# Performance work log

Measured on AMD Instinct MI355X. Metric: run time of the kernel, lower is better.

Reference implementation:

```python
import jax, jax.numpy as jnp
import numpy as np

NUM_HEADS = 8
MODEL_DIM = 1024
SEQ_LEN = 2048


def setup_inputs() -> dict:
    key = jax.random.key(0)
    ks = jax.random.split(key, 9)
    H, D, L = NUM_HEADS, MODEL_DIM, SEQ_LEN
    s_in = 1.0 / np.sqrt(D)
    s_out = 1.0 / np.sqrt(H * D)
    return {
        "tokens": jax.random.normal(ks[0], (D, L), dtype=jnp.float32),
        "Wq": jax.random.uniform(ks[1], (H * D, D), jnp.float32, -s_in, s_in),
        "bq": jax.random.uniform(ks[2], (H * D,), jnp.float32, -s_in, s_in),
        "Wk": jax.random.uniform(ks[3], (H * D, D), jnp.float32, -s_in, s_in),
        "bk": jax.random.uniform(ks[4], (H * D,), jnp.float32, -s_in, s_in),
        "Wv": jax.random.uniform(ks[5], (H * D, D), jnp.float32, -s_in, s_in),
        "bv": jax.random.uniform(ks[6], (H * D,), jnp.float32, -s_in, s_in),
        "Wo": jax.random.uniform(ks[7], (D, H * D), jnp.float32, -s_out, s_out),
        "bo": jax.random.uniform(ks[8], (D,), jnp.float32, -s_out, s_out),
    }


def _split_heads(x, H, D, L):
    # Faithful to torch: raw .view of contiguous [H*D, L] into (L, H, D),
    # then permute(1, 2, 0) -> (H, D, L). This is a memory reinterpretation,
    # not a transpose, exactly as in the original module.
    return x.reshape(L, H, D).transpose(1, 2, 0)


def reference(tokens, Wq, bq, Wk, bk, Wv, bv, Wo, bo):
    D, L = tokens.shape
    H = Wq.shape[0] // D
    # 1x1 Conv1d == matmul over channel dim
    q = _split_heads(Wq @ tokens + bq[:, None], H, D, L)  # (H, D, L)
    k = _split_heads(Wk @ tokens + bk[:, None], H, D, L)  # (H, D, L)
    v = _split_heads(Wv @ tokens + bv[:, None], H, D, L)  # (H, D, L)
    scores = jnp.einsum("hdl,hdm->hlm", q, k) / np.sqrt(D)  # (H, L, L)
    # torch F.softmax without dim on a 3D tensor -> dim=0 (head axis)
    attn = jax.nn.softmax(scores, axis=0)
    ctx = jnp.einsum("hlm,hdm->hdl", attn, v)  # (H, D, L)
    out = Wo @ ctx.reshape(H * D, L) + bo[:, None]  # (D, L)
    return out
```

## Files before the change

### kernel.cpp

```cpp
#include <hip/hip_runtime.h>

#define SEQL 2048
#define DMODEL 1024
#define HDIM 8192

typedef unsigned short bf16_t;
typedef __attribute__((ext_vector_type(8))) short bf16x8;
typedef __attribute__((ext_vector_type(4))) float f32x4;

__device__ __forceinline__ bf16_t f2bf(float f) {
  unsigned u = __float_as_uint(f);
  u += 0x7fffu + ((u >> 16) & 1u);
  return (bf16_t)(u >> 16);
}
__device__ __forceinline__ float bf2f(bf16_t b) {
  return __uint_as_float(((unsigned)b) << 16);
}
__device__ __forceinline__ void st(bf16_t* p, float v) { *p = f2bf(v); }
__device__ __forceinline__ void st(float* p, float v) { *p = v; }

__global__ __launch_bounds__(256) void cvt_f32_bf16(const float* __restrict__ in,
                                                    bf16_t* __restrict__ out, int n) {
  int i = (blockIdx.x * 256 + threadIdx.x) * 4;
  if (i >= n) return;
  float4 f = *reinterpret_cast<const float4*>(in + i);
  ushort4 u;
  u.x = f2bf(f.x); u.y = f2bf(f.y); u.z = f2bf(f.z); u.w = f2bf(f.w);
  *reinterpret_cast<ushort4*>(out + i) = u;
}

__global__ __launch_bounds__(256) void transpose_cvt(const float* __restrict__ in,
                                                     bf16_t* __restrict__ out) {
  __shared__ float tile[32][33];
  int bx = blockIdx.x * 32;
  int by = blockIdx.y * 32;
  int tx = threadIdx.x, ty = threadIdx.y;
#pragma unroll
  for (int i = ty; i < 32; i += 8)
    tile[i][tx] = in[(size_t)(by + i) * SEQL + bx + tx];
  __syncthreads();
#pragma unroll
  for (int i = ty; i < 32; i += 8)
    out[(size_t)(bx + i) * DMODEL + by + tx] = f2bf(tile[tx][i]);
}

__global__ __launch_bounds__(256) void vsplit_k(const bf16_t* __restrict__ Vm,
                                                bf16_t* __restrict__ Vs) {
  __shared__ bf16_t tile[32][33];
  int h = blockIdx.z, h2 = h >> 1, r = h & 1;
  int m0 = blockIdx.x * 32, d0 = blockIdx.y * 32;
  int tx = threadIdx.x, ty = threadIdx.y;
#pragma unroll
  for (int i = ty; i < 32; i += 8)
    tile[i][tx] = Vm[(size_t)(4 * (m0 + i) + h2) * SEQL + r * DMODEL + d0 + tx];
  __syncthreads();
#pragma unroll
  for (int i = ty; i < 32; i += 8)
    Vs[((size_t)h * DMODEL + d0 + i) * SEQL + m0 + tx] = tile[tx][i];
}

__global__ __launch_bounds__(256) void softmax_heads(bf16_t* __restrict__ S) {
  const size_t HS = (size_t)SEQL * SEQL;
  size_t p = ((size_t)blockIdx.x * 256 + threadIdx.x) * 8;
  float v[8][8];
#pragma unroll
  for (int h = 0; h < 8; ++h) {
    bf16x8 x = *reinterpret_cast<const bf16x8*>(S + h * HS + p);
#pragma unroll
    for (int e = 0; e < 8; ++e) v[h][e] = bf2f((bf16_t)x[e]);
  }
#pragma unroll
  for (int e = 0; e < 8; ++e) {
    float mx = v[0][e];
#pragma unroll
    for (int h = 1; h < 8; ++h) mx = fmaxf(mx, v[h][e]);
    float s = 0.f;
#pragma unroll
    for (int h = 0; h < 8; ++h) { v[h][e] = __expf(v[h][e] - mx); s += v[h][e]; }
    float inv = 1.0f / s;
#pragma unroll
    for (int h = 0; h < 8; ++h) v[h][e] *= inv;
  }
#pragma unroll
  for (int h = 0; h < 8; ++h) {
    bf16x8 x;
#pragma unroll
    for (int e = 0; e < 8; ++e) x[e] = (short)f2bf(v[h][e]);
    *reinterpret_cast<bf16x8*>(S + h * HS + p) = x;
  }
}

__global__ __launch_bounds__(256) void reduce_out(const float* __restrict__ P,
                                                  const float* __restrict__ bo,
                                                  float* __restrict__ out) {
  const size_t NEL = (size_t)DMODEL * SEQL;
  size_t i = ((size_t)blockIdx.x * 256 + threadIdx.x) * 4;
  float4 a = *reinterpret_cast<const float4*>(P + i);
#pragma unroll
  for (int z = 1; z < 8; ++z) {
    float4 b = *reinterpret_cast<const float4*>(P + z * NEL + i);
    a.x += b.x; a.y += b.y; a.z += b.z; a.w += b.w;
  }
  float bias = bo[i / SEQL];
  a.x += bias; a.y += bias; a.z += bias; a.w += bias;
  *reinterpret_cast<float4*>(out + i) = a;
}

template <typename OutT, bool HAS_BIAS>
__global__ __launch_bounds__(512, 2) void gemm256(
    const bf16_t* __restrict__ A, const bf16_t* __restrict__ B,
    OutT* __restrict__ C, const float* __restrict__ bias,
    int M, int N, int K, int lda, int ldb, int ldc,
    long long sA, long long sB, long long sC, float scale, int gx) {
  __shared__ alignas(16) bf16_t As[2][2][128 * 64];
  __shared__ alignas(16) bf16_t Bs[2][2][128 * 64];
  const int z = blockIdx.z;
  A += (long long)z * sA;
  B += (long long)z * sB;
  C += (long long)z * sC;
  const int nwg = gridDim.x;
  const int bid = blockIdx.x;
  const int swz = (nwg & 7) ? bid : ((bid & 7) * (nwg >> 3) + (bid >> 3));
  const int brow = (swz / gx) * 256;
  const int bcol = (swz % gx) * 256;
  const int tid = threadIdx.x;
  const int w = tid >> 6, lane = tid & 63;
  const int fr = lane & 15, fq = lane >> 4;
  const int wr = w >> 2, wc = w & 3;

  int rj[2], cj[2];
#pragma unroll
  for (int j = 0; j < 2; ++j) {
    const int c = (w * 2 + j) * 64 + lane;
    rj[j] = c >> 3;
    cj[j] = ((c & 7) ^ (rj[j] & 7)) << 3;
  }

  auto stageA = [&](int buf, int half, int kk) {
#pragma unroll
    for (int j = 0; j < 2; ++j) {
      const bf16_t* g = A + (size_t)(brow + half * 128 + rj[j]) * lda + kk + cj[j];
      __builtin_amdgcn_global_load_lds(
          (const __attribute__((address_space(1))) void*)g,
          (__attribute__((address_space(3))) void*)(&As[buf][half][(w * 2 + j) * 512]),
          16, 0, 0);
    }
  };
  auto stageB = [&](int buf, int half, int kk) {
#pragma unroll
    for (int j = 0; j < 2; ++j) {
      const bf16_t* g = B + (size_t)(bcol + half * 128 + rj[j]) * ldb + kk + cj[j];
      __builtin_amdgcn_global_load_lds(
          (const __attribute__((address_space(1))) void*)g,
          (__attribute__((address_space(3))) void*)(&Bs[buf][half][(w * 2 + j) * 512]),
          16, 0, 0);
    }
  };

  auto ldA = [&](int buf, int mf, int kk) -> bf16x8 {
    const int rr = mf * 16 + fr;
    return *reinterpret_cast<const bf16x8*>(
        &As[buf][wr][rr * 64 + ((((kk << 2) | fq) ^ (rr & 7)) << 3)]);
  };
  auto ldB = [&](int buf, int nf, int kk) -> bf16x8 {
    const int rr = (wc & 1) * 64 + nf * 16 + fr;
    return *reinterpret_cast<const bf16x8*>(
        &Bs[buf][wc >> 1][rr * 64 + ((((kk << 2) | fq) ^ (rr & 7)) << 3)]);
  };

  f32x4 acc[8][4];
  const f32x4 fzero = {0.f, 0.f, 0.f, 0.f};
#pragma unroll
  for (int m = 0; m < 8; ++m)
#pragma unroll
    for (int n = 0; n < 4; ++n) acc[m][n] = fzero;

  const int NT = K >> 6;
  stageA(0, 0, 0); stageA(0, 1, 0); stageB(0, 0, 0); stageB(0, 1, 0);
  __syncthreads();

  for (int t = 0; t < NT; ++t) {
    const int p = t & 1, q = p ^ 1;
    const int kn = (t + 1) << 6;
    const bool pre = (t + 1 < NT);
    bf16x8 af[4][2], bg[4][2];

    if (pre) { stageA(q, 0, kn); stageA(q, 1, kn); }
#pragma unroll
    for (int mf = 0; mf < 4; ++mf)
#pragma unroll
      for (int kk = 0; kk < 2; ++kk) af[mf][kk] = ldA(p, mf, kk);
#pragma unroll
    for (int nf = 0; nf < 2; ++nf)
#pragma unroll
      for (int kk = 0; kk < 2; ++kk) bg[nf][kk] = ldB(p, nf, kk);
    __builtin_amdgcn_s_setprio(1);
#pragma unroll
    for (int mf = 0; mf < 4; ++mf)
#pragma unroll
      for (int nf = 0; nf < 2; ++nf)
#pragma unroll
        for (int kk = 0; kk < 2; ++kk)
          acc[mf][nf] = __builtin_amdgcn_mfma_f32_16x16x32_bf16(
              af[mf][kk], bg[nf][kk], acc[mf][nf], 0, 0, 0);
    __builtin_amdgcn_s_setprio(0);

    if (pre) { stageB(q, 0, kn); stageB(q, 1, kn); }
#pragma unroll
    for (int nf = 2; nf < 4; ++nf)
#pragma unroll
      for (int kk = 0; kk < 2; ++kk) bg[nf][kk] = ldB(p, nf, kk);
    __builtin_amdgcn_s_setprio(1);
#pragma unroll
    for (int mf = 0; mf < 4; ++mf)
#pragma unroll
      for (int nf = 2; nf < 4; ++nf)
#pragma unroll
        for (int kk = 0; kk < 2; ++kk)
          acc[mf][nf] = __builtin_amdgcn_mfma_f32_16x16x32_bf16(
              af[mf][kk], bg[nf][kk], acc[mf][nf], 0, 0, 0);
    __builtin_amdgcn_s_setprio(0);

#pragma unroll
    for (int mf = 0; mf < 4; ++mf)
#pragma unroll
      for (int kk = 0; kk < 2; ++kk) af[mf][kk] = ldA(p, mf + 4, kk);
    __builtin_amdgcn_s_setprio(1);
#pragma unroll
    for (int mf = 0; mf < 4; ++mf)
#pragma unroll
      for (int nf = 2; nf < 4; ++nf)
#pragma unroll
        for (int kk = 0; kk < 2; ++kk)
          acc[mf + 4][nf] = __builtin_amdgcn_mfma_f32_16x16x32_bf16(
              af[mf][kk], bg[nf][kk], acc[mf + 4][nf], 0, 0, 0);
    __builtin_amdgcn_s_setprio(0);

#pragma unroll
    for (int nf = 0; nf < 2; ++nf)
#pragma unroll
      for (int kk = 0; kk < 2; ++kk) bg[nf][kk] = ldB(p, nf, kk);
    __builtin_amdgcn_s_setprio(1);
#pragma unroll
    for (int mf = 0; mf < 4; ++mf)
#pragma unroll
      for (int nf = 0; nf < 2; ++nf)
#pragma unroll
        for (int kk = 0; kk < 2; ++kk)
          acc[mf + 4][nf] = __builtin_amdgcn_mfma_f32_16x16x32_bf16(
              af[mf][kk], bg[nf][kk], acc[mf + 4][nf], 0, 0, 0);
    __builtin_amdgcn_s_setprio(0);

    if (pre) __syncthreads();
  }

#pragma unroll
  for (int mf = 0; mf < 8; ++mf) {
#pragma unroll
    for (int j = 0; j < 4; ++j) {
      const int orow = brow + wr * 128 + mf * 16 + fq * 4 + j;
      float bvv = 0.f;
      if (HAS_BIAS) bvv = bias[orow];
#pragma unroll
      for (int nf = 0; nf < 4; ++nf) {
        const int ocol = bcol + wc * 64 + nf * 16 + fr;
        st(&C[(size_t)orow * ldc + ocol], acc[mf][nf][j] * scale + bvv);
      }
    }
  }
}

extern "C" void kernel_launch(void* const* d_in, const int* in_sizes, int n_in,
                              void* d_out, int out_size, void* d_ws, size_t ws_size,
                              hipStream_t stream) {
  const float* tokens = (const float*)d_in[0];
  const float* Wq = (const float*)d_in[1];
  const float* bq = (const float*)d_in[2];
  const float* Wk = (const float*)d_in[3];
  const float* bk = (const float*)d_in[4];
  const float* Wv = (const float*)d_in[5];
  const float* bv = (const float*)d_in[6];
  const float* Wo = (const float*)d_in[7];
  const float* bo = (const float*)d_in[8];
  float* out = (float*)d_out;
  char* ws = (char*)d_ws;
  const size_t MB = 1024ull * 1024ull;
  bf16_t* tT = (bf16_t*)(ws + 0);
  bf16_t* Wb = (bf16_t*)(ws + 4 * MB);
  bf16_t* Qm = (bf16_t*)(ws + 20 * MB);
  bf16_t* Km = (bf16_t*)(ws + 52 * MB);
  bf16_t* Vm = (bf16_t*)(ws + 84 * MB);
  bf16_t* Sb = (bf16_t*)(ws + 116 * MB);
  bf16_t* Vs = (bf16_t*)(ws + 20 * MB);
  bf16_t* cT = (bf16_t*)(ws + 52 * MB);
  float* Pp = (float*)(ws + 116 * MB);

  dim3 b256(256);
  dim3 b512(512);
  const int nW = HDIM * DMODEL;

  transpose_cvt<<<dim3(SEQL / 32, DMODEL / 32), dim3(32, 8), 0, stream>>>(tokens, tT);

  cvt_f32_bf16<<<nW / 1024, b256, 0, stream>>>(Wq, Wb, nW);
  gemm256<bf16_t, true><<<dim3(32 * 8, 1, 1), b512, 0, stream>>>(
      Wb, tT, Qm, bq, HDIM, SEQL, DMODEL, DMODEL, DMODEL, SEQL, 0, 0, 0, 1.0f, 8);
  cvt_f32_bf16<<<nW / 1024, b256, 0, stream>>>(Wk, Wb, nW);
  gemm256<bf16_t, true><<<dim3(32 * 8, 1, 1), b512, 0, stream>>>(
      Wb, tT, Km, bk, HDIM, SEQL, DMODEL, DMODEL, DMODEL, SEQL, 0, 0, 0, 1.0f, 8);
  cvt_f32_bf16<<<nW / 1024, b256, 0, stream>>>(Wv, Wb, nW);
  gemm256<bf16_t, true><<<dim3(32 * 8, 1, 1), b512, 0, stream>>>(
      Wb, tT, Vm, bv, HDIM, SEQL, DMODEL, DMODEL, DMODEL, SEQL, 0, 0, 0, 1.0f, 8);

  gemm256<bf16_t, false><<<dim3(8 * 8, 1, 8), b512, 0, stream>>>(
      Qm, Km, Sb, nullptr, SEQL, SEQL, DMODEL, HDIM, HDIM, SEQL,
      1024, 1024, (long long)SEQL * SEQL, 0.03125f, 8);

  softmax_heads<<<(SEQL * SEQL / 8) / 256, b256, 0, stream>>>(Sb);

  vsplit_k<<<dim3(SEQL / 32, DMODEL / 32, 8), dim3(32, 8), 0, stream>>>(Vm, Vs);

  gemm256<bf16_t, false><<<dim3(8 * 4, 1, 8), b512, 0, stream>>>(
      Sb, Vs, cT, nullptr, SEQL, DMODEL, SEQL, SEQL, SEQL, HDIM,
      (long long)SEQL * SEQL, (long long)DMODEL * SEQL, DMODEL, 1.0f, 4);

  cvt_f32_bf16<<<nW / 1024, b256, 0, stream>>>(Wo, Wb, nW);
  gemm256<float, false><<<dim3(4 * 8, 1, 8), b512, 0, stream>>>(
      Wb, cT, Pp, nullptr, DMODEL, SEQL, 1024, HDIM, HDIM, SEQL,
      1024, 1024, (long long)DMODEL * SEQL, 1.0f, 8);
  reduce_out<<<(DMODEL * SEQL / 4) / 256, b256, 0, stream>>>(Pp, bo, out);
}
```

Before: 422.7 us.

## Switch GEMM mainloop to triple-buffered K=32 tiles with explicit vmcnt waits

Replaces the double-buffered K=64 LDS pipeline with a three-stage ring of K=32 tiles. Each iteration now prefetches two stages ahead and syncs with a partial s_waitcnt vmcnt plus a raw s_barrier instead of __syncthreads. The LDS layout and XOR swizzle change to 32-element rows. The goal is to hide global-to-LDS latency better and cut barrier stalls, at the cost of twice as many loop iterations and barriers per K and more fragile hand-written wait counts.

```diff
diff --git a/kernel.cpp b/kernel.cpp
--- a/kernel.cpp
+++ b/kernel.cpp
@@ -112,8 +112,8 @@
     OutT* __restrict__ C, const float* __restrict__ bias,
     int M, int N, int K, int lda, int ldb, int ldc,
     long long sA, long long sB, long long sC, float scale, int gx) {
-  __shared__ alignas(16) bf16_t As[2][2][128 * 64];
-  __shared__ alignas(16) bf16_t Bs[2][2][128 * 64];
+  __shared__ alignas(16) bf16_t As[3][256 * 32];
+  __shared__ alignas(16) bf16_t Bs[3][256 * 32];
   const int z = blockIdx.z;
   A += (long long)z * sA;
   B += (long long)z * sB;
@@ -128,44 +128,42 @@
   const int fr = lane & 15, fq = lane >> 4;
   const int wr = w >> 2, wc = w & 3;
 
-  int rj[2], cj[2];
+  int rw[2], co[2];
 #pragma unroll
   for (int j = 0; j < 2; ++j) {
-    const int c = (w * 2 + j) * 64 + lane;
-    rj[j] = c >> 3;
-    cj[j] = ((c & 7) ^ (rj[j] & 7)) << 3;
-  }
-
-  auto stageA = [&](int buf, int half, int kk) {
+    const int c = w * 128 + j * 64 + lane;
+    rw[j] = c >> 2;
+    co[j] = ((c & 3) ^ ((rw[j] >> 1) & 3)) << 3;
+  }
+
+  auto STAGE = [&](int buf, int kk) {
 #pragma unroll
     for (int j = 0; j < 2; ++j) {
-      const bf16_t* g = A + (size_t)(brow + half * 128 + rj[j]) * lda + kk + cj[j];
+      const bf16_t* g = A + (size_t)(brow + rw[j]) * lda + kk + co[j];
       __builtin_amdgcn_global_load_lds(
           (const __attribute__((address_space(1))) void*)g,
-          (__attribute__((address_space(3))) void*)(&As[buf][half][(w * 2 + j) * 512]),
+          (__attribute__((address_space(3))) void*)(&As[buf][w * 1024 + j * 512]),
           16, 0, 0);
     }
-  };
-  auto stageB = [&](int buf, int half, int kk) {
 #pragma unroll
     for (int j = 0; j < 2; ++j) {
-      const bf16_t* g = B + (size_t)(bcol + half * 128 + rj[j]) * ldb + kk + cj[j];
+      const bf16_t* g = B + (size_t)(bcol + rw[j]) * ldb + kk + co[j];
       __builtin_amdgcn_global_load_lds(
           (const __attribute__((address_space(1))) void*)g,
-          (__attribute__((address_space(3))) void*)(&Bs[buf][half][(w * 2 + j) * 512]),
+          (__attribute__((address_space(3))) void*)(&Bs[buf][w * 1024 + j * 512]),
           16, 0, 0);
     }
   };
 
-  auto ldA = [&](int buf, int mf, int kk) -> bf16x8 {
-    const int rr = mf * 16 + fr;
+  auto ldA = [&](int buf, int mf) -> bf16x8 {
+    const int rr = wr * 128 + mf * 16 + fr;
     return *reinterpret_cast<const bf16x8*>(
-        &As[buf][wr][rr * 64 + ((((kk << 2) | fq) ^ (rr & 7)) << 3)]);
+        &As[buf][rr * 32 + ((fq ^ ((rr >> 1) & 3)) << 3)]);
   };
-  auto ldB = [&](int buf, int nf, int kk) -> bf16x8 {
-    const int rr = (wc & 1) * 64 + nf * 16 + fr;
+  auto ldB = [&](int buf, int nf) -> bf16x8 {
+    const int rr = wc * 64 + nf * 16 + fr;
     return *reinterpret_cast<const bf16x8*>(
-        &Bs[buf][wc >> 1][rr * 64 + ((((kk << 2) | fq) ^ (rr & 7)) << 3)]);
+        &Bs[buf][rr * 32 + ((fq ^ ((rr >> 1) & 3)) << 3)]);
   };
 
   f32x4 acc[8][4];
@@ -175,83 +173,46 @@
 #pragma unroll
     for (int n = 0; n < 4; ++n) acc[m][n] = fzero;
 
-  const int NT = K >> 6;
-  stageA(0, 0, 0); stageA(0, 1, 0); stageB(0, 0, 0); stageB(0, 1, 0);
-  __syncthreads();
-
+  const int NT = K >> 5;
+
+  STAGE(0, 0);
+  STAGE(1, 32);
+  asm volatile("s_waitcnt vmcnt(4)" ::: "memory");
+  __builtin_amdgcn_sched_barrier(0);
+  __builtin_amdgcn_s_barrier();
+  __builtin_amdgcn_sched_barrier(0);
+
+  int p = 0;
   for (int t = 0; t < NT; ++t) {
-    const int p = t & 1, q = p ^ 1;
-    const int kn = (t + 1) << 6;
-    const bool pre = (t + 1 < NT);
-    bf16x8 af[4][2], bg[4][2];
-
-    if (pre) { stageA(q, 0, kn); stageA(q, 1, kn); }
-#pragma unroll
-    for (int mf = 0; mf < 4; ++mf)
-#pragma unroll
-      for (int kk = 0; kk < 2; ++kk) af[mf][kk] = ldA(p, mf, kk);
-#pragma unroll
-    for (int nf = 0; nf < 2; ++nf)
-#pragma unroll
-      for (int kk = 0; kk < 2; ++kk) bg[nf][kk] = ldB(p, nf, kk);
+    int sb = p + 2; if (sb >= 3) sb -= 3;
+    const bool pre = (t + 2 < NT);
+    if (pre) STAGE(sb, (t + 2) << 5);
+
+    bf16x8 af[8], bg[4];
+#pragma unroll
+    for (int mf = 0; mf < 8; ++mf) af[mf] = ldA(p, mf);
+#pragma unroll
+    for (int nf = 0; nf < 4; ++nf) bg[nf] = ldB(p, nf);
     __builtin_amdgcn_s_setprio(1);
 #pragma unroll
-    for (int mf = 0; mf < 4; ++mf)
-#pragma unroll
-      for (int nf = 0; nf < 2; ++nf)
-#pragma unroll
-        for (int kk = 0; kk < 2; ++kk)
-          acc[mf][nf] = __builtin_amdgcn_mfma_f32_16x16x32_bf16(
-              af[mf][kk], bg[nf][kk], acc[mf][nf], 0, 0, 0);
+    for (int mf = 0; mf < 8; ++mf)
+#pragma unroll
+      for (int nf = 0; nf < 4; ++nf)
+        acc[mf][nf] = __builtin_amdgcn_mfma_f32_16x16x32_bf16(
+            af[mf], bg[nf], acc[mf][nf], 0, 0, 0);
     __builtin_amdgcn_s_setprio(0);
 
-    if (pre) { stageB(q, 0, kn); stageB(q, 1, kn); }
-#pragma unroll
-    for (int nf = 2; nf < 4; ++nf)
-#pragma unroll
-      for (int kk = 0; kk < 2; ++kk) bg[nf][kk] = ldB(p, nf, kk);
-    __builtin_amdgcn_s_setprio(1);
-#pragma unroll
-    for (int mf = 0; mf < 4; ++mf)
-#pragma unroll
-      for (int nf = 2; nf < 4; ++nf)
-#pragma unroll
-        for (int kk = 0; kk < 2; ++kk)
-          acc[mf][nf] = __builtin_amdgcn_mfma_f32_16x16x32_bf16(
-              af[mf][kk], bg[nf][kk], acc[mf][nf], 0, 0, 0);
-    __builtin_amdgcn_s_setprio(0);
-
-#pragma unroll
-    for (int mf = 0; mf < 4; ++mf)
-#pragma unroll
-      for (int kk = 0; kk < 2; ++kk) af[mf][kk] = ldA(p, mf + 4, kk);
-    __builtin_amdgcn_s_setprio(1);
-#pragma unroll
-    for (int mf = 0; mf < 4; ++mf)
-#pragma unroll
-      for (int nf = 2; nf < 4; ++nf)
-#pragma unroll
-        for (int kk = 0; kk < 2; ++kk)
-          acc[mf + 4][nf] = __builtin_amdgcn_mfma_f32_16x16x32_bf16(
-              af[mf][kk], bg[nf][kk], acc[mf + 4][nf], 0, 0, 0);
-    __builtin_amdgcn_s_setprio(0);
-
-#pragma unroll
-    for (int nf = 0; nf < 2; ++nf)
-#pragma unroll
-      for (int kk = 0; kk < 2; ++kk) bg[nf][kk] = ldB(p, nf, kk);
-    __builtin_amdgcn_s_setprio(1);
-#pragma unroll
-    for (int mf = 0; mf < 4; ++mf)
-#pragma unroll
-      for (int nf = 0; nf < 2; ++nf)
-#pragma unroll
-        for (int kk = 0; kk < 2; ++kk)
-          acc[mf + 4][nf] = __builtin_amdgcn_mfma_f32_16x16x32_bf16(
-              af[mf][kk], bg[nf][kk], acc[mf + 4][nf], 0, 0, 0);
-    __builtin_amdgcn_s_setprio(0);
-
-    if (pre) __syncthreads();
+    __builtin_amdgcn_sched_barrier(0);
+    if (pre) {
+      asm volatile("s_waitcnt vmcnt(4)" ::: "memory");
+    } else {
+      asm volatile("s_waitcnt vmcnt(0)" ::: "memory");
+    }
+    __builtin_amdgcn_sched_barrier(0);
+    __builtin_amdgcn_s_barrier();
+    __builtin_amdgcn_sched_barrier(0);
+
+    ++p; if (p >= 3) p = 0;
   }
 
 #pragma unroll
```

Result: slower. 470.3 us (+11.3%).

## Stage GEMM epilogues through LDS and fuse V head-split transpose into V projection

Applied to the files above, without the earlier changes.

Replaces the scattered per-element global stores in the GEMM epilogue with an LDS-staged tile that is written out in 16-byte vector stores, in bf16 and fp32 variants. The V projection GEMM gets a third epilogue that writes its output already in the head-split transposed layout, so the separate vsplit_k kernel and its extra read/write of V are removed. Shared memory grows to a single 144 KB buffer, which may reduce occupancy below the two blocks per CU the launch bounds request, and the extra barriers add some epilogue latency.

```diff
diff --git a/kernel.cpp b/kernel.cpp
--- a/kernel.cpp
+++ b/kernel.cpp
@@ -16,8 +16,6 @@
 __device__ __forceinline__ float bf2f(bf16_t b) {
   return __uint_as_float(((unsigned)b) << 16);
 }
-__device__ __forceinline__ void st(bf16_t* p, float v) { *p = f2bf(v); }
-__device__ __forceinline__ void st(float* p, float v) { *p = v; }
 
 __global__ __launch_bounds__(256) void cvt_f32_bf16(const float* __restrict__ in,
                                                     bf16_t* __restrict__ out, int n) {
@@ -44,21 +42,6 @@
     out[(size_t)(bx + i) * DMODEL + by + tx] = f2bf(tile[tx][i]);
 }
 
-__global__ __launch_bounds__(256) void vsplit_k(const bf16_t* __restrict__ Vm,
-                                                bf16_t* __restrict__ Vs) {
-  __shared__ bf16_t tile[32][33];
-  int h = blockIdx.z, h2 = h >> 1, r = h & 1;
-  int m0 = blockIdx.x * 32, d0 = blockIdx.y * 32;
-  int tx = threadIdx.x, ty = threadIdx.y;
-#pragma unroll
-  for (int i = ty; i < 32; i += 8)
-    tile[i][tx] = Vm[(size_t)(4 * (m0 + i) + h2) * SEQL + r * DMODEL + d0 + tx];
-  __syncthreads();
-#pragma unroll
-  for (int i = ty; i < 32; i += 8)
-    Vs[((size_t)h * DMODEL + d0 + i) * SEQL + m0 + tx] = tile[tx][i];
-}
-
 __global__ __launch_bounds__(256) void softmax_heads(bf16_t* __restrict__ S) {
   const size_t HS = (size_t)SEQL * SEQL;
   size_t p = ((size_t)blockIdx.x * 256 + threadIdx.x) * 8;
@@ -106,14 +89,15 @@
   *reinterpret_cast<float4*>(out + i) = a;
 }
 
-template <typename OutT, bool HAS_BIAS>
+template <typename OutT, int EPI, bool HAS_BIAS>
 __global__ __launch_bounds__(512, 2) void gemm256(
     const bf16_t* __restrict__ A, const bf16_t* __restrict__ B,
     OutT* __restrict__ C, const float* __restrict__ bias,
     int M, int N, int K, int lda, int ldb, int ldc,
     long long sA, long long sB, long long sC, float scale, int gx) {
-  __shared__ alignas(16) bf16_t As[2][2][128 * 64];
-  __shared__ alignas(16) bf16_t Bs[2][2][128 * 64];
+  __shared__ alignas(16) char smem[147456];
+  auto* As = reinterpret_cast<bf16_t(*)[2][8192]>(smem);
+  auto* Bs = reinterpret_cast<bf16_t(*)[2][8192]>(smem + 65536);
   const int z = blockIdx.z;
   A += (long long)z * sA;
   B += (long long)z * sB;
@@ -254,18 +238,81 @@
     if (pre) __syncthreads();
   }
 
-#pragma unroll
-  for (int mf = 0; mf < 8; ++mf) {
-#pragma unroll
-    for (int j = 0; j < 4; ++j) {
-      const int orow = brow + wr * 128 + mf * 16 + fq * 4 + j;
-      float bvv = 0.f;
-      if (HAS_BIAS) bvv = bias[orow];
-#pragma unroll
-      for (int nf = 0; nf < 4; ++nf) {
-        const int ocol = bcol + wc * 64 + nf * 16 + fr;
-        st(&C[(size_t)orow * ldc + ocol], acc[mf][nf][j] * scale + bvv);
+  __syncthreads();
+
+  if constexpr (EPI == 0) {
+    bf16_t* Ct = (bf16_t*)smem;
+#pragma unroll
+    for (int mf = 0; mf < 8; ++mf)
+#pragma unroll
+      for (int j = 0; j < 4; ++j) {
+        const int orow = wr * 128 + mf * 16 + fq * 4 + j;
+        float bvv = HAS_BIAS ? bias[brow + orow] : 0.f;
+#pragma unroll
+        for (int nf = 0; nf < 4; ++nf)
+          Ct[orow * 264 + wc * 64 + nf * 16 + fr] = f2bf(acc[mf][nf][j] * scale + bvv);
       }
+    __syncthreads();
+#pragma unroll
+    for (int i = 0; i < 16; ++i) {
+      const int c = tid + i * 512;
+      const int row = c >> 5, ch = c & 31;
+      *reinterpret_cast<bf16x8*>(&C[(size_t)(brow + row) * ldc + bcol + ch * 8]) =
+          *reinterpret_cast<const bf16x8*>(smem + row * 528 + ch * 16);
+    }
+  } else if constexpr (EPI == 1) {
+    float* Cf = (float*)smem;
+#pragma unroll
+    for (int h = 0; h < 2; ++h) {
+      if (wr == h) {
+#pragma unroll
+        for (int mf = 0; mf < 8; ++mf)
+#pragma unroll
+          for (int j = 0; j < 4; ++j) {
+            const int orow = mf * 16 + fq * 4 + j;
+            float bvv = HAS_BIAS ? bias[brow + h * 128 + orow] : 0.f;
+#pragma unroll
+            for (int nf = 0; nf < 4; ++nf)
+              Cf[orow * 264 + wc * 64 + nf * 16 + fr] = acc[mf][nf][j] * scale + bvv;
+          }
+      }
+      __syncthreads();
+#pragma unroll
+      for (int i = 0; i < 16; ++i) {
+        const int c = tid + i * 512;
+        const int row = c >> 6, ch = c & 63;
+        *reinterpret_cast<float4*>(&C[(size_t)(brow + h * 128 + row) * ldc + bcol + ch * 4]) =
+            *reinterpret_cast<const float4*>(smem + row * 1056 + ch * 16);
+      }
+      __syncthreads();
+    }
+  } else {
+    bf16_t* Vt = (bf16_t*)smem;
+#pragma unroll
+    for (int mf = 0; mf < 8; ++mf)
+#pragma unroll
+      for (int j = 0; j < 4; ++j) {
+        const int i = wr * 128 + mf * 16 + fq * 4 + j;
+        const int mloc = i >> 2;
+        float bvv = HAS_BIAS ? bias[brow + i] : 0.f;
+#pragma unroll
+        for (int nf = 0; nf < 4; ++nf) {
+          const int dloc = wc * 64 + nf * 16 + fr;
+          Vt[(j * 256 + dloc) * 72 + mloc] = f2bf(acc[mf][nf][j] * scale + bvv);
+        }
+      }
+    __syncthreads();
+    const int r_ = bcol >> 10, d0 = bcol & 1023, m0 = brow >> 2;
+#pragma unroll
+    for (int sIt = 0; sIt < 2; ++sIt) {
+      const int s = tid + sIt * 512;
+      const int h2 = s >> 8, dloc = s & 255;
+      const bf16_t* src = Vt + (h2 * 256 + dloc) * 72;
+      bf16_t* dst = (bf16_t*)C + ((size_t)(2 * h2 + r_) * DMODEL + d0 + dloc) * SEQL + m0;
+#pragma unroll
+      for (int qq = 0; qq < 8; ++qq)
+        *reinterpret_cast<bf16x8*>(dst + qq * 8) =
+            *reinterpret_cast<const bf16x8*>(src + qq * 8);
     }
   }
 }
@@ -289,10 +336,9 @@
   bf16_t* Wb = (bf16_t*)(ws + 4 * MB);
   bf16_t* Qm = (bf16_t*)(ws + 20 * MB);
   bf16_t* Km = (bf16_t*)(ws + 52 * MB);
-  bf16_t* Vm = (bf16_t*)(ws + 84 * MB);
+  bf16_t* Vs = (bf16_t*)(ws + 84 * MB);
   bf16_t* Sb = (bf16_t*)(ws + 116 * MB);
-  bf16_t* Vs = (bf16_t*)(ws + 20 * MB);
-  bf16_t* cT = (bf16_t*)(ws + 52 * MB);
+  bf16_t* cT = (bf16_t*)(ws + 20 * MB);
   float* Pp = (float*)(ws + 116 * MB);
 
   dim3 b256(256);
@@ -302,29 +348,27 @@
   transpose_cvt<<<dim3(SEQL / 32, DMODEL / 32), dim3(32, 8), 0, stream>>>(tokens, tT);
 
   cvt_f32_bf16<<<nW / 1024, b256, 0, stream>>>(Wq, Wb, nW);
-  gemm256<bf16_t, true><<<dim3(32 * 8, 1, 1), b512, 0, stream>>>(
+  gemm256<bf16_t, 0, true><<<dim3(32 * 8, 1, 1), b512, 0, stream>>>(
       Wb, tT, Qm, bq, HDIM, SEQL, DMODEL, DMODEL, DMODEL, SEQL, 0, 0, 0, 1.0f, 8);
   cvt_f32_bf16<<<nW / 1024, b256, 0, stream>>>(Wk, Wb, nW);
-  gemm256<bf16_t, true><<<dim3(32 * 8, 1, 1), b512, 0, stream>>>(
+  gemm256<bf16_t, 0, true><<<dim3(32 * 8, 1, 1), b512, 0, stream>>>(
       Wb, tT, Km, bk, HDIM, SEQL, DMODEL, DMODEL, DMODEL, SEQL, 0, 0, 0, 1.0f, 8);
   cvt_f32_bf16<<<nW / 1024, b256, 0, stream>>>(Wv, Wb, nW);
-  gemm256<bf16_t, true><<<dim3(32 * 8, 1, 1), b512, 0, stream>>>(
-      Wb, tT, Vm, bv, HDIM, SEQL, DMODEL, DMODEL, DMODEL, SEQL, 0, 0, 0, 1.0f, 8);
-
-  gemm256<bf16_t, false><<<dim3(8 * 8, 1, 8), b512, 0, stream>>>(
+  gemm256<bf16_t, 2, true><<<dim3(32 * 8, 1, 1), b512, 0, stream>>>(
+      Wb, tT, Vs, bv, HDIM, SEQL, DMODEL, DMODEL, DMODEL, SEQL, 0, 0, 0, 1.0f, 8);
+
+  gemm256<bf16_t, 0, false><<<dim3(8 * 8, 1, 8), b512, 0, stream>>>(
       Qm, Km, Sb, nullptr, SEQL, SEQL, DMODEL, HDIM, HDIM, SEQL,
       1024, 1024, (long long)SEQL * SEQL, 0.03125f, 8);
 
   softmax_heads<<<(SEQL * SEQL / 8) / 256, b256, 0, stream>>>(Sb);
 
-  vsplit_k<<<dim3(SEQL / 32, DMODEL / 32, 8), dim3(32, 8), 0, stream>>>(Vm, Vs);
-
-  gemm256<bf16_t, false><<<dim3(8 * 4, 1, 8), b512, 0, stream>>>(
+  gemm256<bf16_t, 0, false><<<dim3(8 * 4, 1, 8), b512, 0, stream>>>(
       Sb, Vs, cT, nullptr, SEQL, DMODEL, SEQL, SEQL, SEQL, HDIM,
       (long long)SEQL * SEQL, (long long)DMODEL * SEQL, DMODEL, 1.0f, 4);
 
   cvt_f32_bf16<<<nW / 1024, b256, 0, stream>>>(Wo, Wb, nW);
-  gemm256<float, false><<<dim3(4 * 8, 1, 8), b512, 0, stream>>>(
+  gemm256<float, 1, false><<<dim3(4 * 8, 1, 8), b512, 0, stream>>>(
       Wb, cT, Pp, nullptr, DMODEL, SEQL, 1024, HDIM, HDIM, SEQL,
       1024, 1024, (long long)DMODEL * SEQL, 1.0f, 8);
   reduce_out<<<(DMODEL * SEQL / 4) / 256, b256, 0, stream>>>(Pp, bo, out);
```

New measurement: 369.2 us. 1.14x faster.
